# Optimization experiments

Hardware: AMD Instinct MI355X
Metric: run time of the kernel (lower is better)

The kernel has to match this reference:

```python
import jax, jax.numpy as jnp
import numpy as np

RADIUS = 2  # matches LGA(radius=2)


def setup_inputs() -> dict:
    key = jax.random.key(0)
    k1, k2 = jax.random.split(key)
    N, C, H, W = 4, 32, 384, 768
    K = 2 * RADIUS + 1
    input1 = jax.random.normal(k1, (N, C, H, W), dtype=jnp.float32)
    input2 = jax.random.uniform(k2, (N, K * K, H, W), dtype=jnp.float32)
    return {"input1": input1, "input2": input2}


def reference(input1, input2):
    # Local Guided Aggregation (GANet LGA):
    # out[n,c,h,w] = sum_{i,j in (2r+1)^2} input1[n,c,h+i-r,w+j-r] * input2[n,i*K+j,h,w]
    # Per-pixel 5x5 filter shared across channels; zero padding at borders.
    r = RADIUS
    K = 2 * r + 1
    N, C, H, W = input1.shape
    padded = jnp.pad(input1, ((0, 0), (0, 0), (r, r), (r, r)))
    out = jnp.zeros_like(input1)
    for i in range(K):
        for j in range(K):
            # shifted window [N,C,H,W] times per-pixel tap weight [N,1,H,W]
            out = out + padded[:, :, i:i + H, j:j + W] * input2[:, i * K + j][:, None, :, :]
    return out
```

## Files before the change

kernel.cpp:

```cpp
#include <hip/hip_runtime.h>


#define N_DIM 4
#define C_DIM 32
#define H_DIM 384
#define W_DIM 768
#define TH 4
#define TW 256
#define LROWS (TH + 4)
#define LW 260

__global__ __launch_bounds__(256, 3)
void lga_kernel(const float* __restrict__ in1,
                const float* __restrict__ in2,
                float* __restrict__ out) {
    __shared__ float lds[LROWS * LW];

    const int tid = threadIdx.x;
    const int tx  = tid & 63;
    const int ty  = tid >> 6;
    const int w0  = blockIdx.x * TW;
    const int h0  = blockIdx.y * TH;
    const int n   = blockIdx.z;

    const int h   = h0 + ty;
    const int wb  = w0 + 4 * tx;

    float4 wt[25];
    const float* w_src = in2 + ((size_t)n * 25) * (H_DIM * W_DIM)
                             + (size_t)h * W_DIM + wb;
#pragma unroll
    for (int t = 0; t < 25; ++t) {
        wt[t] = *(const float4*)(w_src + (size_t)t * (H_DIM * W_DIM));
    }

    const float* in1_n = in1 + (size_t)n * C_DIM * H_DIM * W_DIM;
    float*       out_n = out + (size_t)n * C_DIM * H_DIM * W_DIM;

    for (int c = 0; c < C_DIM; ++c) {
        const float* src = in1_n + (size_t)c * (H_DIM * W_DIM);

        for (int idx = tid; idx < LROWS * 65; idx += 256) {
            const int row = idx / 65;
            const int c4  = idx - row * 65;
            const int gh  = h0 - 2 + row;
            const int g   = w0 - 2 + 4 * c4;
            float4 v;
            if ((unsigned)gh < H_DIM && g >= 0 && g + 3 < W_DIM) {
                const float* p = src + gh * W_DIM + g;
                const float2 a = *(const float2*)p;
                const float2 b = *(const float2*)(p + 2);
                v = make_float4(a.x, a.y, b.x, b.y);
            } else {
                const bool rok = (unsigned)gh < H_DIM;
                const float* prow = src + gh * W_DIM;
                v.x = (rok && (unsigned)(g + 0) < W_DIM) ? prow[g + 0] : 0.f;
                v.y = (rok && (unsigned)(g + 1) < W_DIM) ? prow[g + 1] : 0.f;
                v.z = (rok && (unsigned)(g + 2) < W_DIM) ? prow[g + 2] : 0.f;
                v.w = (rok && (unsigned)(g + 3) < W_DIM) ? prow[g + 3] : 0.f;
            }
            *(float4*)&lds[row * LW + 4 * c4] = v;
        }
        __syncthreads();

        float acc0 = 0.f, acc1 = 0.f, acc2 = 0.f, acc3 = 0.f;
#pragma unroll
        for (int i = 0; i < 5; ++i) {
            const float* lrow = &lds[(ty + i) * LW + 4 * tx];
            const float4 A = *(const float4*)lrow;
            const float4 B = *(const float4*)(lrow + 4);
            const float win[8] = {A.x, A.y, A.z, A.w, B.x, B.y, B.z, B.w};
#pragma unroll
            for (int j = 0; j < 5; ++j) {
                const float4 wv = wt[5 * i + j];
                acc0 += wv.x * win[j + 0];
                acc1 += wv.y * win[j + 1];
                acc2 += wv.z * win[j + 2];
                acc3 += wv.w * win[j + 3];
            }
        }

        *(float4*)(out_n + (size_t)c * (H_DIM * W_DIM) + (size_t)h * W_DIM + wb)
            = make_float4(acc0, acc1, acc2, acc3);
        __syncthreads();
    }
}

extern "C" void kernel_launch(void* const* d_in, const int* in_sizes, int n_in,
                              void* d_out, int out_size, void* d_ws, size_t ws_size,
                              hipStream_t stream) {
    const float* in1 = (const float*)d_in[0];
    const float* in2 = (const float*)d_in[1];
    float* out = (float*)d_out;
    dim3 grid(W_DIM / TW, H_DIM / TH, N_DIM);
    lga_kernel<<<grid, 256, 0, stream>>>(in1, in2, out);
}
```

Measured before the change: 453.2 us.

## Replace LDS tiling with direct per-wave global loads and flat wave mapping

Removes the shared-memory staging tile and both block barriers per channel. Each wave now handles one 256-wide row segment and reads its 5x8 input window straight from global memory, relying on L1/L2 caches to serve the reuse across neighbouring rows and lanes. Block-to-work mapping becomes a flat wave index. This avoids LDS traffic and sync stalls, but it issues more global load instructions, including unaligned float2 halo loads, per channel.

```diff
diff --git a/kernel.cpp b/kernel.cpp
--- a/kernel.cpp
+++ b/kernel.cpp
@@ -5,84 +5,69 @@
 #define C_DIM 32
 #define H_DIM 384
 #define W_DIM 768
-#define TH 4
-#define TW 256
-#define LROWS (TH + 4)
-#define LW 260
+#define HW (H_DIM * W_DIM)
 
 __global__ __launch_bounds__(256, 3)
 void lga_kernel(const float* __restrict__ in1,
                 const float* __restrict__ in2,
                 float* __restrict__ out) {
-    __shared__ float lds[LROWS * LW];
-
-    const int tid = threadIdx.x;
-    const int tx  = tid & 63;
-    const int ty  = tid >> 6;
-    const int w0  = blockIdx.x * TW;
-    const int h0  = blockIdx.y * TH;
-    const int n   = blockIdx.z;
-
-    const int h   = h0 + ty;
-    const int wb  = w0 + 4 * tx;
+    const int wave = (int)((blockIdx.x * blockDim.x + threadIdx.x) >> 6);
+    const int lane = threadIdx.x & 63;
+    const int rw   = wave % 3;
+    const int hrow = (wave / 3) % H_DIM;
+    const int n    = wave / (3 * H_DIM);
+    const int wb   = rw * 256 + 4 * lane;
 
     float4 wt[25];
-    const float* w_src = in2 + ((size_t)n * 25) * (H_DIM * W_DIM)
-                             + (size_t)h * W_DIM + wb;
+    const float* wsrc = in2 + (size_t)n * 25 * HW + (size_t)hrow * W_DIM + wb;
 #pragma unroll
-    for (int t = 0; t < 25; ++t) {
-        wt[t] = *(const float4*)(w_src + (size_t)t * (H_DIM * W_DIM));
-    }
+    for (int t = 0; t < 25; ++t)
+        wt[t] = *(const float4*)(wsrc + (size_t)t * HW);
 
-    const float* in1_n = in1 + (size_t)n * C_DIM * H_DIM * W_DIM;
-    float*       out_n = out + (size_t)n * C_DIM * H_DIM * W_DIM;
+    const bool lok = (wb != 0);
+    const bool rko = (wb != W_DIM - 4);
+    bool rvalid[5];
+#pragma unroll
+    for (int i = 0; i < 5; ++i)
+        rvalid[i] = (unsigned)(hrow - 2 + i) < (unsigned)H_DIM;
+
+    const float* src = in1 + (size_t)n * C_DIM * HW + (size_t)hrow * W_DIM + wb;
+    float*       dst = out + (size_t)n * C_DIM * HW + (size_t)hrow * W_DIM + wb;
 
     for (int c = 0; c < C_DIM; ++c) {
-        const float* src = in1_n + (size_t)c * (H_DIM * W_DIM);
-
-        for (int idx = tid; idx < LROWS * 65; idx += 256) {
-            const int row = idx / 65;
-            const int c4  = idx - row * 65;
-            const int gh  = h0 - 2 + row;
-            const int g   = w0 - 2 + 4 * c4;
-            float4 v;
-            if ((unsigned)gh < H_DIM && g >= 0 && g + 3 < W_DIM) {
-                const float* p = src + gh * W_DIM + g;
-                const float2 a = *(const float2*)p;
-                const float2 b = *(const float2*)(p + 2);
-                v = make_float4(a.x, a.y, b.x, b.y);
-            } else {
-                const bool rok = (unsigned)gh < H_DIM;
-                const float* prow = src + gh * W_DIM;
-                v.x = (rok && (unsigned)(g + 0) < W_DIM) ? prow[g + 0] : 0.f;
-                v.y = (rok && (unsigned)(g + 1) < W_DIM) ? prow[g + 1] : 0.f;
-                v.z = (rok && (unsigned)(g + 2) < W_DIM) ? prow[g + 2] : 0.f;
-                v.w = (rok && (unsigned)(g + 3) < W_DIM) ? prow[g + 3] : 0.f;
-            }
-            *(float4*)&lds[row * LW + 4 * c4] = v;
-        }
-        __syncthreads();
-
-        float acc0 = 0.f, acc1 = 0.f, acc2 = 0.f, acc3 = 0.f;
+        float win[5][8];
 #pragma unroll
         for (int i = 0; i < 5; ++i) {
-            const float* lrow = &lds[(ty + i) * LW + 4 * tx];
-            const float4 A = *(const float4*)lrow;
-            const float4 B = *(const float4*)(lrow + 4);
-            const float win[8] = {A.x, A.y, A.z, A.w, B.x, B.y, B.z, B.w};
+            const float* p = src + (i - 2) * W_DIM;
+            float2 L = make_float2(0.f, 0.f);
+            float2 R = make_float2(0.f, 0.f);
+            float4 M = make_float4(0.f, 0.f, 0.f, 0.f);
+            if (rvalid[i]) {
+                M = *(const float4*)p;
+                if (lok) L = *(const float2*)(p - 2);
+                if (rko) R = *(const float2*)(p + 4);
+            }
+            win[i][0] = L.x; win[i][1] = L.y;
+            win[i][2] = M.x; win[i][3] = M.y; win[i][4] = M.z; win[i][5] = M.w;
+            win[i][6] = R.x; win[i][7] = R.y;
+        }
+
+        float a0 = 0.f, a1 = 0.f, a2 = 0.f, a3 = 0.f;
+#pragma unroll
+        for (int i = 0; i < 5; ++i) {
 #pragma unroll
             for (int j = 0; j < 5; ++j) {
                 const float4 wv = wt[5 * i + j];
-                acc0 += wv.x * win[j + 0];
-                acc1 += wv.y * win[j + 1];
-                acc2 += wv.z * win[j + 2];
-                acc3 += wv.w * win[j + 3];
+                a0 += wv.x * win[i][j + 0];
+                a1 += wv.y * win[i][j + 1];
+                a2 += wv.z * win[i][j + 2];
+                a3 += wv.w * win[i][j + 3];
             }
         }
 
-        *(float4*)(out_n + (size_t)c * (H_DIM * W_DIM) + (size_t)h * W_DIM + wb)
-            = make_float4(acc0, acc1, acc2, acc3);
-        __syncthreads();
+        *(float4*)dst = make_float4(a0, a1, a2, a3);
+        src += HW;
+        dst += HW;
     }
 }
 
@@ -92,6 +77,6 @@
     const float* in1 = (const float*)d_in[0];
     const float* in2 = (const float*)d_in[1];
     float* out = (float*)d_out;
-    dim3 grid(W_DIM / TW, H_DIM / TH, N_DIM);
-    lga_kernel<<<grid, 256, 0, stream>>>(in1, in2, out);
+    const int total_threads = N_DIM * H_DIM * (W_DIM / 4);
+    lga_kernel<<<total_threads / 256, 256, 0, stream>>>(in1, in2, out);
 }
```

Result: no change. 458.4 us (+1.2%).
